# Optimization experiments

Measured on AMD Instinct MI355X. Metric: run time of the kernel, lower is better.

The kernel has to match this reference:

```python
import jax, jax.numpy as jnp
import numpy as np

D = 1024       # hidden_size
H = 16         # num_heads
DH = D // H    # d_keys = d_values = 64
FF = int(D * 2.0)  # mlp hidden
EPS = 1e-6


def _ln(t):
    # LayerNorm, elementwise_affine=False
    mu = jnp.mean(t, axis=-1, keepdims=True)
    var = jnp.mean((t - mu) ** 2, axis=-1, keepdims=True)
    return (t - mu) * jax.lax.rsqrt(var + EPS)


def setup_inputs() -> dict:
    key = jax.random.key(0)
    ks = jax.random.split(key, 16)
    B, L = 2, 2048
    s = 0.02
    return {
        "x": jax.random.normal(ks[0], (B, L, D), jnp.float32),
        "c": jax.random.normal(ks[1], (B, 1, D), jnp.float32),
        "Wq": jax.random.normal(ks[2], (D, D), jnp.float32) * s,
        "bq": jnp.zeros((D,), jnp.float32),
        "Wk": jax.random.normal(ks[3], (D, D), jnp.float32) * s,
        "bk": jnp.zeros((D,), jnp.float32),
        "Wv": jax.random.normal(ks[4], (D, D), jnp.float32) * s,
        "bv": jnp.zeros((D,), jnp.float32),
        "Wo": jax.random.normal(ks[5], (D, D), jnp.float32) * s,
        "bo": jnp.zeros((D,), jnp.float32),
        "W1": jax.random.normal(ks[6], (D, FF), jnp.float32) * s,
        "b1": jnp.zeros((FF,), jnp.float32),
        "W2": jax.random.normal(ks[7], (FF, D), jnp.float32) * s,
        "b2": jnp.zeros((D,), jnp.float32),
        "Wada": jax.random.normal(ks[8], (D, 6 * D), jnp.float32) * s,
        "bada": jnp.zeros((6 * D,), jnp.float32),
    }


def reference(x, c, Wq, bq, Wk, bk, Wv, bv, Wo, bo, W1, b1, W2, b2, Wada, bada):
    B, L, _ = x.shape
    # adaLN-Zero modulation params (dropout layers act as identity in eval)
    ada = jax.nn.silu(c) @ Wada + bada  # [B,1,6D]
    shift_msa, scale_msa, gate_msa, shift_mlp, scale_mlp, gate_mlp = jnp.split(ada, 6, axis=-1)

    # --- attention branch ---
    h = _ln(x) * (1.0 + scale_msa) + shift_msa
    q = (h @ Wq + bq).reshape(B, L, H, DH)
    k = (h @ Wk + bk).reshape(B, L, H, DH)
    v = (h @ Wv + bv).reshape(B, L, H, DH)
    scale = 1.0 / np.sqrt(DH).astype(np.float32)
    scores = jnp.einsum('blhe,bshe->bhls', q, k)  # full LxL scores, as in source
    A = jax.nn.softmax(scale * scores, axis=-1)
    out = jnp.einsum('bhls,bshd->blhd', A, v)     # [B,L,H,DH]
    # mix=True: transpose(2,1) then view(B,L,-1) -> head/position mixing reshape
    out = jnp.transpose(out, (0, 2, 1, 3)).reshape(B, L, H * DH)
    x = x + gate_msa * (out @ Wo + bo)

    # --- MLP branch (exact GELU: nn.GELU() passed as act_layer) ---
    h2 = _ln(x) * (1.0 + scale_mlp) + shift_mlp
    m = jax.nn.gelu(h2 @ W1 + b1, approximate=False) @ W2 + b2
    return x + gate_mlp * m
```

## Files before the change

kernel.cpp:

```cpp
#include <hip/hip_runtime.h>
#include <hip/hip_bf16.h>

typedef unsigned short ushort_t;
typedef __bf16 bf16x8 __attribute__((ext_vector_type(8)));
typedef float f32x4 __attribute__((ext_vector_type(4)));

typedef unsigned int u32;
typedef u32 __attribute__((address_space(1))) global_u32;
typedef u32 __attribute__((address_space(3))) lds_u32;

#define D_ 1024
#define L_ 2048
#define B_ 2
#define H_ 16
#define DH_ 64
#define FF_ 2048
#define ADA_ 6144
#define BHL_ (B_ * H_ * L_)

#define MFMA __builtin_amdgcn_mfma_f32_16x16x32_bf16

__device__ __forceinline__ ushort_t f2bf(float f) {
    union { float f; u32 u; } v; v.f = f;
    u32 r = v.u + 0x7fffu + ((v.u >> 16) & 1u);
    return (ushort_t)(r >> 16);
}

__device__ __forceinline__ u32 pk_bf16(float a, float b) {
    float2 f; f.x = a; f.y = b;
    __hip_bfloat162 t = __float22bfloat162_rn(f);
    union { __hip_bfloat162 b2; u32 u; } v; v.b2 = t; return v.u;
}

__device__ __forceinline__ void llds16(const ushort_t* src, ushort_t* dst) {
    __builtin_amdgcn_global_load_lds((global_u32*)src, (lds_u32*)dst, 16, 0, 0);
}

__global__ void transpose_w_all(
    const float* __restrict__ Wq, const float* __restrict__ Wk,
    const float* __restrict__ Wv, const float* __restrict__ Wo,
    const float* __restrict__ W1, const float* __restrict__ W2,
    ushort_t* __restrict__ Wqkv, ushort_t* __restrict__ Wo_t,
    ushort_t* __restrict__ W1_t, ushort_t* __restrict__ W2_t) {
    __shared__ float tile[64][65];
    int id = blockIdx.x;
    const float* W; ushort_t* Wt; int K, N, ntx, lid;
    if (id < 1024) {
        int which = id >> 8; lid = id & 255; K = 1024; N = 1024; ntx = 16;
        W  = which == 0 ? Wq : which == 1 ? Wk : which == 2 ? Wv : Wo;
        Wt = which == 3 ? Wo_t : Wqkv + (size_t)which * 1024 * 1024;
    } else if (id < 1536) {
        lid = id - 1024; W = W1; Wt = W1_t; K = 1024; N = 2048; ntx = 32;
    } else {
        lid = id - 1536; W = W2; Wt = W2_t; K = 2048; N = 1024; ntx = 16;
    }
    int n0 = (lid % ntx) * 64, k0 = (lid / ntx) * 64;
    int t = threadIdx.x;
    for (int p = 0; p < 4; ++p) {
        int k = p * 16 + (t >> 4), nn = (t & 15) * 4;
        float4 v = *(const float4*)(W + (size_t)(k0 + k) * N + n0 + nn);
        tile[k][nn] = v.x; tile[k][nn + 1] = v.y; tile[k][nn + 2] = v.z; tile[k][nn + 3] = v.w;
    }
    __syncthreads();
    for (int p = 0; p < 4; ++p) {
        int n = p * 16 + (t >> 4), kk = (t & 15) * 4;
        ushort4 o;
        o.x = f2bf(tile[kk][n]); o.y = f2bf(tile[kk + 1][n]);
        o.z = f2bf(tile[kk + 2][n]); o.w = f2bf(tile[kk + 3][n]);
        *(ushort4*)(Wt + (size_t)(n0 + n) * K + k0 + kk) = o;
    }
}

__global__ void transpose_v(const ushort_t* __restrict__ V, ushort_t* __restrict__ Vt) {
    __shared__ ushort_t tile[64][72];
    int bh = blockIdx.y, l0 = blockIdx.x * 64;
    const ushort_t* Vb = V + ((size_t)bh * L_ + l0) * DH_;
    ushort_t* Vtb = Vt + (size_t)bh * DH_ * L_;
    int t = threadIdx.x;
    for (int p = 0; p < 2; ++p) {
        int i = p * 32 + (t >> 3), d0 = (t & 7) * 8;
        ushort4 v0 = *(const ushort4*)(Vb + (size_t)i * DH_ + d0);
        ushort4 v1 = *(const ushort4*)(Vb + (size_t)i * DH_ + d0 + 4);
        tile[d0 + 0][i] = v0.x; tile[d0 + 1][i] = v0.y; tile[d0 + 2][i] = v0.z; tile[d0 + 3][i] = v0.w;
        tile[d0 + 4][i] = v1.x; tile[d0 + 5][i] = v1.y; tile[d0 + 6][i] = v1.z; tile[d0 + 7][i] = v1.w;
    }
    __syncthreads();
    for (int p = 0; p < 2; ++p) {
        int dh = p * 32 + (t >> 3), j0 = (t & 7) * 8;
        ushort4 o0, o1;
        o0.x = tile[dh][j0 + 0]; o0.y = tile[dh][j0 + 1]; o0.z = tile[dh][j0 + 2]; o0.w = tile[dh][j0 + 3];
        o1.x = tile[dh][j0 + 4]; o1.y = tile[dh][j0 + 5]; o1.z = tile[dh][j0 + 6]; o1.w = tile[dh][j0 + 7];
        *(ushort4*)(Vtb + (size_t)dh * L_ + l0 + j0) = o0;
        *(ushort4*)(Vtb + (size_t)dh * L_ + l0 + j0 + 4) = o1;
    }
}

__global__ void ada_gemv(const float* __restrict__ c, const float* __restrict__ Wada,
                         float* __restrict__ partial) {
    int ks = blockIdx.y;
    int j = blockIdx.x * 256 + threadIdx.x;
    __shared__ float s0[64], s1[64];
    if (threadIdx.x < 64) {
        float v = c[ks * 64 + threadIdx.x];
        s0[threadIdx.x] = v / (1.f + __expf(-v));
        v = c[D_ + ks * 64 + threadIdx.x];
        s1[threadIdx.x] = v / (1.f + __expf(-v));
    }
    __syncthreads();
    float a0 = 0.f, a1 = 0.f;
#pragma unroll 8
    for (int d = 0; d < 64; ++d) {
        float w = Wada[(size_t)(ks * 64 + d) * ADA_ + j];
        a0 = fmaf(s0[d], w, a0);
        a1 = fmaf(s1[d], w, a1);
    }
    partial[(size_t)(ks * 2 + 0) * ADA_ + j] = a0;
    partial[(size_t)(ks * 2 + 1) * ADA_ + j] = a1;
}

__global__ void ada_reduce(const float* __restrict__ partial,
                           const float* __restrict__ bada, float* __restrict__ ada) {
    int j = blockIdx.x * 256 + threadIdx.x;
    float a0 = bada[j], a1 = bada[j];
#pragma unroll
    for (int ks = 0; ks < 16; ++ks) {
        a0 += partial[(size_t)(ks * 2 + 0) * ADA_ + j];
        a1 += partial[(size_t)(ks * 2 + 1) * ADA_ + j];
    }
    ada[j] = a0;
    ada[ADA_ + j] = a1;
}

__global__ void ln_mod(const float* __restrict__ x, const float* __restrict__ ada,
                       int so, int co, ushort_t* __restrict__ out) {
    int row = blockIdx.x;
    int b = row >> 11;
    float4 v = ((const float4*)(x + (size_t)row * D_))[threadIdx.x];
    float sum = v.x + v.y + v.z + v.w;
    float sq = v.x * v.x + v.y * v.y + v.z * v.z + v.w * v.w;
    for (int off = 32; off; off >>= 1) { sum += __shfl_down(sum, off); sq += __shfl_down(sq, off); }
    __shared__ float sa[4], sb[4];
    int wave = threadIdx.x >> 6, lane = threadIdx.x & 63;
    if (lane == 0) { sa[wave] = sum; sb[wave] = sq; }
    __syncthreads();
    sum = sa[0] + sa[1] + sa[2] + sa[3];
    sq = sb[0] + sb[1] + sb[2] + sb[3];
    float mean = sum * (1.f / 1024.f);
    float var = sq * (1.f / 1024.f) - mean * mean;
    float rstd = rsqrtf(var + 1e-6f);
    int d = threadIdx.x * 4;
    const float* shf = ada + (size_t)b * ADA_ + so;
    const float* scf = ada + (size_t)b * ADA_ + co;
    uint2 ov;
    ov.x = pk_bf16((v.x - mean) * rstd * (1.f + scf[d + 0]) + shf[d + 0],
                   (v.y - mean) * rstd * (1.f + scf[d + 1]) + shf[d + 1]);
    ov.y = pk_bf16((v.z - mean) * rstd * (1.f + scf[d + 2]) + shf[d + 2],
                   (v.w - mean) * rstd * (1.f + scf[d + 3]) + shf[d + 3]);
    *(uint2*)(out + (size_t)row * D_ + d) = ov;
}

struct EpiArgs {
    const float* bias0; const float* bias1; const float* bias2;
    ushort_t* o0; ushort_t* o1; ushort_t* o2;
    const float* resid; const float* gate;
    float* fout;
};

template <int EPI>
__device__ __forceinline__ void epi_store(float v, int m, int n, int N, const EpiArgs& e) {
    if (EPI == 0) {
        int which = n >> 10, cc = n & 1023;
        const float* bias = which == 0 ? e.bias0 : which == 1 ? e.bias1 : e.bias2;
        ushort_t* ob = which == 0 ? e.o0 : which == 1 ? e.o1 : e.o2;
        v += bias[cc];
        if (which == 0) v *= 0.18033688f;
        int b = m >> 11, l = m & 2047, h = cc >> 6, dh = cc & 63;
        ob[(((size_t)(b * H_ + h) * L_) + l) * DH_ + dh] = f2bf(v);
    } else if (EPI == 1) {
        v += e.bias0[n];
        v = 0.5f * v * (1.f + erff(v * 0.70710678118f));
        e.o0[(size_t)m * N + n] = f2bf(v);
    } else {
        int b = m >> 11;
        e.fout[(size_t)m * N + n] =
            e.resid[(size_t)m * N + n] + e.gate[(size_t)b * ADA_ + n] * (v + e.bias0[n]);
    }
}

template <int EPI>
__device__ __forceinline__ void st4(const f32x4& cc, int mb, int n, int N, const EpiArgs& e) {
#pragma unroll
    for (int r = 0; r < 4; ++r) epi_store<EPI>(cc[r], mb + r, n, N, e);
}

template <int EPI>
__global__ __launch_bounds__(256, 2) void gemm_bt(
    const ushort_t* __restrict__ A, const ushort_t* __restrict__ Bt,
    int M, int N, int K, EpiArgs e) {
    __shared__ ushort_t As[128 * 64];
    __shared__ ushort_t Bs[128 * 64];
    int m0 = blockIdx.x * 128, n0 = blockIdx.y * 128;
    int tid = threadIdx.x, wave = tid >> 6, lane = tid & 63;
    int quad = lane >> 4, lc = lane & 15;
    int wm = (wave & 1) * 64, wn = (wave >> 1) * 64;
    int srow = lane >> 3, sg = lane & 7;
    int sw = lc & 7;

    const ushort_t* stp[8];
    ushort_t* stl[8];
#pragma unroll
    for (int i = 0; i < 8; ++i) {
        int chunk = wave * 8 + i;
        int c = chunk & 15;
        int row = c * 8 + srow;
        stp[i] = (chunk < 16 ? A + (size_t)(m0 + row) * K
                             : Bt + (size_t)(n0 + row) * K) + (sg ^ srow) * 8;
        stl[i] = (chunk < 16 ? As : Bs) + c * 512 + lane * 8;
    }

    f32x4 c00 = {}, c01 = {}, c02 = {}, c03 = {};
    f32x4 c10 = {}, c11 = {}, c12 = {}, c13 = {};
    f32x4 c20 = {}, c21 = {}, c22 = {}, c23 = {};
    f32x4 c30 = {}, c31 = {}, c32 = {}, c33 = {};

    for (int k0 = 0; k0 < K; k0 += 64) {
#pragma unroll
        for (int i = 0; i < 8; ++i) { llds16(stp[i], stl[i]); stp[i] += 64; }
        __syncthreads();
#pragma unroll
        for (int kk = 0; kk < 2; ++kk) {
            int off = ((kk * 4 + quad) ^ sw) * 8;
            bf16x8 a0 = *(const bf16x8*)&As[(wm +  0 + lc) * 64 + off];
            bf16x8 a1 = *(const bf16x8*)&As[(wm + 16 + lc) * 64 + off];
            bf16x8 a2 = *(const bf16x8*)&As[(wm + 32 + lc) * 64 + off];
            bf16x8 a3 = *(const bf16x8*)&As[(wm + 48 + lc) * 64 + off];
            bf16x8 b0 = *(const bf16x8*)&Bs[(wn +  0 + lc) * 64 + off];
            bf16x8 b1 = *(const bf16x8*)&Bs[(wn + 16 + lc) * 64 + off];
            bf16x8 b2 = *(const bf16x8*)&Bs[(wn + 32 + lc) * 64 + off];
            bf16x8 b3 = *(const bf16x8*)&Bs[(wn + 48 + lc) * 64 + off];
            c00 = MFMA(a0, b0, c00, 0, 0, 0); c01 = MFMA(a0, b1, c01, 0, 0, 0);
            c02 = MFMA(a0, b2, c02, 0, 0, 0); c03 = MFMA(a0, b3, c03, 0, 0, 0);
            c10 = MFMA(a1, b0, c10, 0, 0, 0); c11 = MFMA(a1, b1, c11, 0, 0, 0);
            c12 = MFMA(a1, b2, c12, 0, 0, 0); c13 = MFMA(a1, b3, c13, 0, 0, 0);
            c20 = MFMA(a2, b0, c20, 0, 0, 0); c21 = MFMA(a2, b1, c21, 0, 0, 0);
            c22 = MFMA(a2, b2, c22, 0, 0, 0); c23 = MFMA(a2, b3, c23, 0, 0, 0);
            c30 = MFMA(a3, b0, c30, 0, 0, 0); c31 = MFMA(a3, b1, c31, 0, 0, 0);
            c32 = MFMA(a3, b2, c32, 0, 0, 0); c33 = MFMA(a3, b3, c33, 0, 0, 0);
        }
        __syncthreads();
    }

    int mb = m0 + wm + quad * 4, nb = n0 + wn + lc;
    st4<EPI>(c00, mb +  0, nb +  0, N, e); st4<EPI>(c01, mb +  0, nb + 16, N, e);
    st4<EPI>(c02, mb +  0, nb + 32, N, e); st4<EPI>(c03, mb +  0, nb + 48, N, e);
    st4<EPI>(c10, mb + 16, nb +  0, N, e); st4<EPI>(c11, mb + 16, nb + 16, N, e);
    st4<EPI>(c12, mb + 16, nb + 32, N, e); st4<EPI>(c13, mb + 16, nb + 48, N, e);
    st4<EPI>(c20, mb + 32, nb +  0, N, e); st4<EPI>(c21, mb + 32, nb + 16, N, e);
    st4<EPI>(c22, mb + 32, nb + 32, N, e); st4<EPI>(c23, mb + 32, nb + 48, N, e);
    st4<EPI>(c30, mb + 48, nb +  0, N, e); st4<EPI>(c31, mb + 48, nb + 16, N, e);
    st4<EPI>(c32, mb + 48, nb + 32, N, e); st4<EPI>(c33, mb + 48, nb + 48, N, e);
}

template <int EPI>
__global__ __launch_bounds__(256, 2) void gemm_bt64(
    const ushort_t* __restrict__ A, const ushort_t* __restrict__ Bt,
    int M, int N, int K, EpiArgs e) {
    __shared__ ushort_t As[64 * 64];
    __shared__ ushort_t Bs[128 * 64];
    int m0 = blockIdx.x * 64, n0 = blockIdx.y * 128;
    int tid = threadIdx.x, wave = tid >> 6, lane = tid & 63;
    int quad = lane >> 4, lc = lane & 15;
    int wn = wave * 32;
    int srow = lane >> 3, sg = lane & 7;
    int sw = lc & 7;

    const ushort_t* stp[6];
    ushort_t* stl[6];
#pragma unroll
    for (int i = 0; i < 6; ++i) {
        int chunk = wave * 6 + i;
        if (chunk < 8) {
            int row = chunk * 8 + srow;
            stp[i] = A + (size_t)(m0 + row) * K + (sg ^ srow) * 8;
            stl[i] = &As[chunk * 512 + lane * 8];
        } else {
            int c = chunk - 8;
            int row = c * 8 + srow;
            stp[i] = Bt + (size_t)(n0 + row) * K + (sg ^ srow) * 8;
            stl[i] = &Bs[c * 512 + lane * 8];
        }
    }

    f32x4 c00 = {}, c01 = {};
    f32x4 c10 = {}, c11 = {};
    f32x4 c20 = {}, c21 = {};
    f32x4 c30 = {}, c31 = {};

    for (int k0 = 0; k0 < K; k0 += 64) {
#pragma unroll
        for (int i = 0; i < 6; ++i) { llds16(stp[i], stl[i]); stp[i] += 64; }
        __syncthreads();
#pragma unroll
        for (int kk = 0; kk < 2; ++kk) {
            int off = ((kk * 4 + quad) ^ sw) * 8;
            bf16x8 a0 = *(const bf16x8*)&As[( 0 + lc) * 64 + off];
            bf16x8 a1 = *(const bf16x8*)&As[(16 + lc) * 64 + off];
            bf16x8 a2 = *(const bf16x8*)&As[(32 + lc) * 64 + off];
            bf16x8 a3 = *(const bf16x8*)&As[(48 + lc) * 64 + off];
            bf16x8 b0 = *(const bf16x8*)&Bs[(wn +  0 + lc) * 64 + off];
            bf16x8 b1 = *(const bf16x8*)&Bs[(wn + 16 + lc) * 64 + off];
            c00 = MFMA(a0, b0, c00, 0, 0, 0); c01 = MFMA(a0, b1, c01, 0, 0, 0);
            c10 = MFMA(a1, b0, c10, 0, 0, 0); c11 = MFMA(a1, b1, c11, 0, 0, 0);
            c20 = MFMA(a2, b0, c20, 0, 0, 0); c21 = MFMA(a2, b1, c21, 0, 0, 0);
            c30 = MFMA(a3, b0, c30, 0, 0, 0); c31 = MFMA(a3, b1, c31, 0, 0, 0);
        }
        __syncthreads();
    }

    int mb = m0 + quad * 4, nb = n0 + wn + lc;
    st4<EPI>(c00, mb +  0, nb + 0, N, e); st4<EPI>(c01, mb +  0, nb + 16, N, e);
    st4<EPI>(c10, mb + 16, nb + 0, N, e); st4<EPI>(c11, mb + 16, nb + 16, N, e);
    st4<EPI>(c20, mb + 32, nb + 0, N, e); st4<EPI>(c21, mb + 32, nb + 16, N, e);
    st4<EPI>(c30, mb + 48, nb + 0, N, e); st4<EPI>(c31, mb + 48, nb + 16, N, e);
}

__global__ __launch_bounds__(256, 2) void attn(
    const ushort_t* __restrict__ Q, const ushort_t* __restrict__ Kx,
    const ushort_t* __restrict__ Vt,
    ushort_t* __restrict__ Op0, ushort_t* __restrict__ Op1,
    ushort_t* __restrict__ Op2, ushort_t* __restrict__ Op3,
    float* __restrict__ lsum) {
    __shared__ ushort_t Ks[128 * 64];
    __shared__ ushort_t Vs[64 * 128];
    int id = blockIdx.x;
    int bh = ((id & 7) << 2) + ((id >> 3) & 3);
    int quarter = (id >> 5) & 3;
    int qt = id >> 7;
    const ushort_t* Qg = Q + ((size_t)bh * L_ + qt * 128) * DH_;
    const ushort_t* Kg = Kx + (size_t)bh * L_ * DH_;
    const ushort_t* Vg = Vt + (size_t)bh * DH_ * L_;
    int tid = threadIdx.x, wave = tid >> 6, lane = tid & 63;
    int quad = lane >> 4, lc = lane & 15;
    int sw = lc & 7;
    int srow = lane >> 3, sg = lane & 7;

    const ushort_t* stp[8];
    ushort_t* stl[8];
    int stinc;
    if (wave < 2) {
        stinc = 128 * DH_;
#pragma unroll
        for (int i = 0; i < 8; ++i) {
            int chunk = wave * 8 + i;
            int slot = chunk * 8 + srow;
            int s5 = slot & 31;
            int sig = (slot & ~31) + ((s5 & 15) >> 2) * 8 + (s5 & 3) + (s5 >> 4) * 4;
            stp[i] = Kg + (size_t)(quarter * 512 + sig) * DH_ + (sg ^ srow) * 8;
            stl[i] = &Ks[chunk * 512 + lane * 8];
        }
    } else {
        stinc = 128;
#pragma unroll
        for (int i = 0; i < 8; ++i) {
            int c2 = (wave - 2) * 8 + i;
            int row = c2 * 4 + (lane >> 4);
            int g = (lane & 15) ^ (row & 15);
            stp[i] = Vg + (size_t)row * L_ + quarter * 512 + g * 8;
            stl[i] = &Vs[c2 * 512 + lane * 8];
        }
    }

    const ushort_t* qp = Qg + (size_t)(wave * 32 + lc) * DH_ + quad * 8;
    bf16x8 q00 = *(const bf16x8*)(qp);
    bf16x8 q01 = *(const bf16x8*)(qp + 32);
    bf16x8 q10 = *(const bf16x8*)(qp + 16 * DH_);
    bf16x8 q11 = *(const bf16x8*)(qp + 16 * DH_ + 32);

    union { u32 u[4]; bf16x8 v; } ones;
    ones.u[0] = ones.u[1] = ones.u[2] = ones.u[3] = 0x3F803F80u;

    f32x4 o00 = {}, o01 = {}, o02 = {}, o03 = {};
    f32x4 o10 = {}, o11 = {}, o12 = {}, o13 = {};
    f32x4 osum0 = {}, osum1 = {};

    for (int t = 0; t < 4; ++t) {
#pragma unroll
        for (int i = 0; i < 8; ++i) { llds16(stp[i], stl[i]); stp[i] += stinc; }
        __syncthreads();

        f32x4 s[2][8];
        __builtin_amdgcn_s_setprio(1);
#pragma unroll
        for (int kk = 0; kk < 2; ++kk) {
            int off = ((kk * 4 + quad) ^ sw) * 8;
            bf16x8 aq0 = kk == 0 ? q00 : q01;
            bf16x8 aq1 = kk == 0 ? q10 : q11;
#pragma unroll
            for (int ni = 0; ni < 8; ++ni) {
                bf16x8 bk = *(const bf16x8*)&Ks[(ni * 16 + lc) * 64 + off];
                if (kk == 0) {
                    f32x4 z = {0.f, 0.f, 0.f, 0.f};
                    s[0][ni] = MFMA(bk, aq0, z, 0, 0, 0);
                    s[1][ni] = MFMA(bk, aq1, z, 0, 0, 0);
                } else {
                    s[0][ni] = MFMA(bk, aq0, s[0][ni], 0, 0, 0);
                    s[1][ni] = MFMA(bk, aq1, s[1][ni], 0, 0, 0);
                }
            }
        }
        __builtin_amdgcn_s_setprio(0);

        u32 px[2][8], py[2][8];
#pragma unroll
        for (int pi = 0; pi < 2; ++pi) {
#pragma unroll
            for (int ni = 0; ni < 8; ++ni) {
                float p0 = __builtin_amdgcn_exp2f(s[pi][ni][0]);
                float p1 = __builtin_amdgcn_exp2f(s[pi][ni][1]);
                float p2 = __builtin_amdgcn_exp2f(s[pi][ni][2]);
                float p3 = __builtin_amdgcn_exp2f(s[pi][ni][3]);
                px[pi][ni] = pk_bf16(p0, p1);
                py[pi][ni] = pk_bf16(p2, p3);
            }
        }

        __builtin_amdgcn_s_setprio(1);
#pragma unroll
        for (int kk = 0; kk < 4; ++kk) {
            int gq = kk * 4 + quad;
            bf16x8 bv0 = *(const bf16x8*)&Vs[( 0 + lc) * 128 + ((gq ^ lc) * 8)];
            bf16x8 bv1 = *(const bf16x8*)&Vs[(16 + lc) * 128 + ((gq ^ lc) * 8)];
            bf16x8 bv2 = *(const bf16x8*)&Vs[(32 + lc) * 128 + ((gq ^ lc) * 8)];
            bf16x8 bv3 = *(const bf16x8*)&Vs[(48 + lc) * 128 + ((gq ^ lc) * 8)];
            union { u32 u[4]; bf16x8 v; } a0, a1;
            a0.u[0] = px[0][2 * kk]; a0.u[1] = py[0][2 * kk];
            a0.u[2] = px[0][2 * kk + 1]; a0.u[3] = py[0][2 * kk + 1];
            a1.u[0] = px[1][2 * kk]; a1.u[1] = py[1][2 * kk];
            a1.u[2] = px[1][2 * kk + 1]; a1.u[3] = py[1][2 * kk + 1];
            o00 = MFMA(a0.v, bv0, o00, 0, 0, 0); o01 = MFMA(a0.v, bv1, o01, 0, 0, 0);
            o02 = MFMA(a0.v, bv2, o02, 0, 0, 0); o03 = MFMA(a0.v, bv3, o03, 0, 0, 0);
            o10 = MFMA(a1.v, bv0, o10, 0, 0, 0); o11 = MFMA(a1.v, bv1, o11, 0, 0, 0);
            o12 = MFMA(a1.v, bv2, o12, 0, 0, 0); o13 = MFMA(a1.v, bv3, o13, 0, 0, 0);
            osum0 = MFMA(a0.v, ones.v, osum0, 0, 0, 0);
            osum1 = MFMA(a1.v, ones.v, osum1, 0, 0, 0);
        }
        __builtin_amdgcn_s_setprio(0);
        __syncthreads();
    }

    ushort_t* Op = quarter == 0 ? Op0 : quarter == 1 ? Op1 : quarter == 2 ? Op2 : Op3;
#pragma unroll
    for (int pi = 0; pi < 2; ++pi) {
#pragma unroll
        for (int nio = 0; nio < 4; ++nio) {
            const f32x4& ov = pi == 0 ? (nio == 0 ? o00 : nio == 1 ? o01 : nio == 2 ? o02 : o03)
                                      : (nio == 0 ? o10 : nio == 1 ? o11 : nio == 2 ? o12 : o13);
#pragma unroll
            for (int r = 0; r < 4; ++r) {
                int row = qt * 128 + wave * 32 + pi * 16 + quad * 4 + r;
                Op[((size_t)bh * L_ + row) * DH_ + nio * 16 + lc] = f2bf(ov[r]);
            }
        }
    }
    if (lc == 0) {
        int base = qt * 128 + wave * 32 + quad * 4;
#pragma unroll
        for (int r = 0; r < 4; ++r) {
            lsum[(size_t)quarter * BHL_ + (size_t)bh * L_ + base + r] = osum0[r];
            lsum[(size_t)quarter * BHL_ + (size_t)bh * L_ + base + 16 + r] = osum1[r];
        }
    }
}

__global__ void attn_merge(const ushort_t* __restrict__ Op0,
                           const ushort_t* __restrict__ Op1,
                           const ushort_t* __restrict__ Op2,
                           const ushort_t* __restrict__ Op3,
                           const float* __restrict__ lsum,
                           ushort_t* __restrict__ O) {
    int gid = blockIdx.x * 256 + threadIdx.x;
    int row = gid >> 3, j = gid & 7;
    float inv = 1.f / (lsum[row] + lsum[BHL_ + row] +
                       lsum[2 * BHL_ + row] + lsum[3 * BHL_ + row]);
    bf16x8 v0 = *(const bf16x8*)(Op0 + (size_t)row * DH_ + j * 8);
    bf16x8 v1 = *(const bf16x8*)(Op1 + (size_t)row * DH_ + j * 8);
    bf16x8 v2 = *(const bf16x8*)(Op2 + (size_t)row * DH_ + j * 8);
    bf16x8 v3 = *(const bf16x8*)(Op3 + (size_t)row * DH_ + j * 8);
    uint4 o;
    float r0, r1;
#pragma unroll
    for (int k = 0; k < 4; ++k) {
        r0 = ((float)v0[2 * k] + (float)v1[2 * k] + (float)v2[2 * k] + (float)v3[2 * k]) * inv;
        r1 = ((float)v0[2 * k + 1] + (float)v1[2 * k + 1] + (float)v2[2 * k + 1] + (float)v3[2 * k + 1]) * inv;
        ((u32*)&o)[k] = pk_bf16(r0, r1);
    }
    *(uint4*)(O + (size_t)row * DH_ + j * 8) = o;
}

extern "C" void kernel_launch(void* const* d_in, const int* in_sizes, int n_in,
                              void* d_out, int out_size, void* d_ws, size_t ws_size,
                              hipStream_t stream) {
    (void)in_sizes; (void)n_in; (void)out_size; (void)ws_size;
    const float* x    = (const float*)d_in[0];
    const float* c    = (const float*)d_in[1];
    const float* Wq   = (const float*)d_in[2];
    const float* bq   = (const float*)d_in[3];
    const float* Wk   = (const float*)d_in[4];
    const float* bk   = (const float*)d_in[5];
    const float* Wv   = (const float*)d_in[6];
    const float* bv   = (const float*)d_in[7];
    const float* Wo   = (const float*)d_in[8];
    const float* bo   = (const float*)d_in[9];
    const float* W1   = (const float*)d_in[10];
    const float* b1   = (const float*)d_in[11];
    const float* W2   = (const float*)d_in[12];
    const float* b2   = (const float*)d_in[13];
    const float* Wada = (const float*)d_in[14];
    const float* bada = (const float*)d_in[15];

    char* w = (char*)d_ws;
    float*    ada  = (float*)(w + 0);
    ushort_t* Wqkv = (ushort_t*)(w + 49152);
    ushort_t* Wo_t = (ushort_t*)(w + 6340608);
    ushort_t* W1_t = (ushort_t*)(w + 8437760);
    ushort_t* W2_t = (ushort_t*)(w + 12632064);
    ushort_t* h    = (ushort_t*)(w + 16826368);
    ushort_t* Qb   = (ushort_t*)(w + 25214976);
    ushort_t* Kb   = (ushort_t*)(w + 33603584);
    ushort_t* Vb   = (ushort_t*)(w + 41992192);
    ushort_t* Vtb  = (ushort_t*)(w + 50380800);
    float*    x1   = (float*)(w + 58769408);
    ushort_t* Ob   = Qb;
    ushort_t* m1   = Qb;
    float*    lsb  = (float*)Wqkv;
    float*    adap = (float*)Vtb;
    ushort_t* p2   = (ushort_t*)x1;
    ushort_t* p3   = (ushort_t*)((char*)x1 + 8388608);

    const int M = B_ * L_;

    transpose_w_all<<<2048, 256, 0, stream>>>(Wq, Wk, Wv, Wo, W1, W2,
                                              Wqkv, Wo_t, W1_t, W2_t);

    ada_gemv<<<dim3(24, 16), 256, 0, stream>>>(c, Wada, adap);
    ada_reduce<<<24, 256, 0, stream>>>(adap, bada, ada);
    ln_mod<<<M, 256, 0, stream>>>(x, ada, 0, 1024, h);

    EpiArgs e0 = {bq, bk, bv, Qb, Kb, Vb, nullptr, nullptr, nullptr};
    gemm_bt<0><<<dim3(32, 24), 256, 0, stream>>>(h, Wqkv, M, 3072, D_, e0);

    transpose_v<<<dim3(32, 32), 256, 0, stream>>>(Vb, Vtb);

    attn<<<2048, 256, 0, stream>>>(Qb, Kb, Vtb, Vb, h, p2, p3, lsb);
    attn_merge<<<2048, 256, 0, stream>>>(Vb, h, p2, p3, lsb, Ob);

    EpiArgs e1 = {bo, nullptr, nullptr, nullptr, nullptr, nullptr, x, ada + 2048, x1};
    gemm_bt64<2><<<dim3(64, 8), 256, 0, stream>>>(Ob, Wo_t, M, D_, D_, e1);

    ln_mod<<<M, 256, 0, stream>>>(x1, ada, 3072, 4096, h);

    EpiArgs e2 = {b1, nullptr, nullptr, m1, nullptr, nullptr, nullptr, nullptr, nullptr};
    gemm_bt64<1><<<dim3(64, 16), 256, 0, stream>>>(h, W1_t, M, FF_, D_, e2);

    EpiArgs e3 = {b2, nullptr, nullptr, nullptr, nullptr, nullptr, x1, ada + 5120, (float*)d_out};
    gemm_bt64<2><<<dim3(64, 8), 256, 0, stream>>>(m1, W2_t, M, D_, FF_, e3);
}
```

Before: 321.4 us.

## Write V transposed from QKV GEMM epilogue and drop split-K attention merge

The QKV GEMM epilogue now writes V straight into the transposed [bh, dh, L] layout with 4-wide stores, so the separate transpose_v kernel goes away. Attention no longer splits the key dimension into four quarters with partial outputs and a merge kernel. Each block loops over all 2048 keys and normalizes by the row sum in its own epilogue. This removes two launches and the partial-output and row-sum traffic, but the attention grid shrinks from 2048 to 512 blocks, which lowers parallelism and lengthens each block's serial loop.

```diff
diff --git a/kernel.cpp b/kernel.cpp
--- a/kernel.cpp
+++ b/kernel.cpp
@@ -68,30 +68,6 @@
         o.x = f2bf(tile[kk][n]); o.y = f2bf(tile[kk + 1][n]);
         o.z = f2bf(tile[kk + 2][n]); o.w = f2bf(tile[kk + 3][n]);
         *(ushort4*)(Wt + (size_t)(n0 + n) * K + k0 + kk) = o;
-    }
-}
-
-__global__ void transpose_v(const ushort_t* __restrict__ V, ushort_t* __restrict__ Vt) {
-    __shared__ ushort_t tile[64][72];
-    int bh = blockIdx.y, l0 = blockIdx.x * 64;
-    const ushort_t* Vb = V + ((size_t)bh * L_ + l0) * DH_;
-    ushort_t* Vtb = Vt + (size_t)bh * DH_ * L_;
-    int t = threadIdx.x;
-    for (int p = 0; p < 2; ++p) {
-        int i = p * 32 + (t >> 3), d0 = (t & 7) * 8;
-        ushort4 v0 = *(const ushort4*)(Vb + (size_t)i * DH_ + d0);
-        ushort4 v1 = *(const ushort4*)(Vb + (size_t)i * DH_ + d0 + 4);
-        tile[d0 + 0][i] = v0.x; tile[d0 + 1][i] = v0.y; tile[d0 + 2][i] = v0.z; tile[d0 + 3][i] = v0.w;
-        tile[d0 + 4][i] = v1.x; tile[d0 + 5][i] = v1.y; tile[d0 + 6][i] = v1.z; tile[d0 + 7][i] = v1.w;
-    }
-    __syncthreads();
-    for (int p = 0; p < 2; ++p) {
-        int dh = p * 32 + (t >> 3), j0 = (t & 7) * 8;
-        ushort4 o0, o1;
-        o0.x = tile[dh][j0 + 0]; o0.y = tile[dh][j0 + 1]; o0.z = tile[dh][j0 + 2]; o0.w = tile[dh][j0 + 3];
-        o1.x = tile[dh][j0 + 4]; o1.y = tile[dh][j0 + 5]; o1.z = tile[dh][j0 + 6]; o1.w = tile[dh][j0 + 7];
-        *(ushort4*)(Vtb + (size_t)dh * L_ + l0 + j0) = o0;
-        *(ushort4*)(Vtb + (size_t)dh * L_ + l0 + j0 + 4) = o1;
     }
 }
 
@@ -170,8 +146,8 @@
 __device__ __forceinline__ void epi_store(float v, int m, int n, int N, const EpiArgs& e) {
     if (EPI == 0) {
         int which = n >> 10, cc = n & 1023;
-        const float* bias = which == 0 ? e.bias0 : which == 1 ? e.bias1 : e.bias2;
-        ushort_t* ob = which == 0 ? e.o0 : which == 1 ? e.o1 : e.o2;
+        const float* bias = which == 0 ? e.bias0 : e.bias1;
+        ushort_t* ob = which == 0 ? e.o0 : e.o1;
         v += bias[cc];
         if (which == 0) v *= 0.18033688f;
         int b = m >> 11, l = m & 2047, h = cc >> 6, dh = cc & 63;
@@ -189,6 +165,16 @@
 
 template <int EPI>
 __device__ __forceinline__ void st4(const f32x4& cc, int mb, int n, int N, const EpiArgs& e) {
+    if (EPI == 0 && n >= 2048) {
+        int ccn = n & 1023;
+        float b4 = e.bias2[ccn];
+        int b = mb >> 11, l0 = mb & 2047, h = ccn >> 6, dh = ccn & 63;
+        ushort4 o;
+        o.x = f2bf(cc[0] + b4); o.y = f2bf(cc[1] + b4);
+        o.z = f2bf(cc[2] + b4); o.w = f2bf(cc[3] + b4);
+        *(ushort4*)(e.o2 + ((size_t)(b * H_ + h) * DH_ + dh) * L_ + l0) = o;
+        return;
+    }
 #pragma unroll
     for (int r = 0; r < 4; ++r) epi_store<EPI>(cc[r], mb + r, n, N, e);
 }
@@ -326,16 +312,12 @@
 
 __global__ __launch_bounds__(256, 2) void attn(
     const ushort_t* __restrict__ Q, const ushort_t* __restrict__ Kx,
-    const ushort_t* __restrict__ Vt,
-    ushort_t* __restrict__ Op0, ushort_t* __restrict__ Op1,
-    ushort_t* __restrict__ Op2, ushort_t* __restrict__ Op3,
-    float* __restrict__ lsum) {
+    const ushort_t* __restrict__ Vt, ushort_t* __restrict__ O) {
     __shared__ ushort_t Ks[128 * 64];
     __shared__ ushort_t Vs[64 * 128];
     int id = blockIdx.x;
     int bh = ((id & 7) << 2) + ((id >> 3) & 3);
-    int quarter = (id >> 5) & 3;
-    int qt = id >> 7;
+    int qt = id >> 5;
     const ushort_t* Qg = Q + ((size_t)bh * L_ + qt * 128) * DH_;
     const ushort_t* Kg = Kx + (size_t)bh * L_ * DH_;
     const ushort_t* Vg = Vt + (size_t)bh * DH_ * L_;
@@ -355,7 +337,7 @@
             int slot = chunk * 8 + srow;
             int s5 = slot & 31;
             int sig = (slot & ~31) + ((s5 & 15) >> 2) * 8 + (s5 & 3) + (s5 >> 4) * 4;
-            stp[i] = Kg + (size_t)(quarter * 512 + sig) * DH_ + (sg ^ srow) * 8;
+            stp[i] = Kg + (size_t)sig * DH_ + (sg ^ srow) * 8;
             stl[i] = &Ks[chunk * 512 + lane * 8];
         }
     } else {
@@ -365,7 +347,7 @@
             int c2 = (wave - 2) * 8 + i;
             int row = c2 * 4 + (lane >> 4);
             int g = (lane & 15) ^ (row & 15);
-            stp[i] = Vg + (size_t)row * L_ + quarter * 512 + g * 8;
+            stp[i] = Vg + (size_t)row * L_ + g * 8;
             stl[i] = &Vs[c2 * 512 + lane * 8];
         }
     }
@@ -383,7 +365,7 @@
     f32x4 o10 = {}, o11 = {}, o12 = {}, o13 = {};
     f32x4 osum0 = {}, osum1 = {};
 
-    for (int t = 0; t < 4; ++t) {
+    for (int t = 0; t < 16; ++t) {
 #pragma unroll
         for (int i = 0; i < 8; ++i) { llds16(stp[i], stl[i]); stp[i] += stinc; }
         __syncthreads();
@@ -448,9 +430,12 @@
         __syncthreads();
     }
 
-    ushort_t* Op = quarter == 0 ? Op0 : quarter == 1 ? Op1 : quarter == 2 ? Op2 : Op3;
+    f32x4 inv0, inv1;
+#pragma unroll
+    for (int r = 0; r < 4; ++r) { inv0[r] = 1.f / osum0[r]; inv1[r] = 1.f / osum1[r]; }
 #pragma unroll
     for (int pi = 0; pi < 2; ++pi) {
+        const f32x4& iv = pi == 0 ? inv0 : inv1;
 #pragma unroll
         for (int nio = 0; nio < 4; ++nio) {
             const f32x4& ov = pi == 0 ? (nio == 0 ? o00 : nio == 1 ? o01 : nio == 2 ? o02 : o03)
@@ -458,43 +443,10 @@
 #pragma unroll
             for (int r = 0; r < 4; ++r) {
                 int row = qt * 128 + wave * 32 + pi * 16 + quad * 4 + r;
-                Op[((size_t)bh * L_ + row) * DH_ + nio * 16 + lc] = f2bf(ov[r]);
+                O[((size_t)bh * L_ + row) * DH_ + nio * 16 + lc] = f2bf(ov[r] * iv[r]);
             }
         }
     }
-    if (lc == 0) {
-        int base = qt * 128 + wave * 32 + quad * 4;
-#pragma unroll
-        for (int r = 0; r < 4; ++r) {
-            lsum[(size_t)quarter * BHL_ + (size_t)bh * L_ + base + r] = osum0[r];
-            lsum[(size_t)quarter * BHL_ + (size_t)bh * L_ + base + 16 + r] = osum1[r];
-        }
-    }
-}
-
-__global__ void attn_merge(const ushort_t* __restrict__ Op0,
-                           const ushort_t* __restrict__ Op1,
-                           const ushort_t* __restrict__ Op2,
-                           const ushort_t* __restrict__ Op3,
-                           const float* __restrict__ lsum,
-                           ushort_t* __restrict__ O) {
-    int gid = blockIdx.x * 256 + threadIdx.x;
-    int row = gid >> 3, j = gid & 7;
-    float inv = 1.f / (lsum[row] + lsum[BHL_ + row] +
-                       lsum[2 * BHL_ + row] + lsum[3 * BHL_ + row]);
-    bf16x8 v0 = *(const bf16x8*)(Op0 + (size_t)row * DH_ + j * 8);
-    bf16x8 v1 = *(const bf16x8*)(Op1 + (size_t)row * DH_ + j * 8);
-    bf16x8 v2 = *(const bf16x8*)(Op2 + (size_t)row * DH_ + j * 8);
-    bf16x8 v3 = *(const bf16x8*)(Op3 + (size_t)row * DH_ + j * 8);
-    uint4 o;
-    float r0, r1;
-#pragma unroll
-    for (int k = 0; k < 4; ++k) {
-        r0 = ((float)v0[2 * k] + (float)v1[2 * k] + (float)v2[2 * k] + (float)v3[2 * k]) * inv;
-        r1 = ((float)v0[2 * k + 1] + (float)v1[2 * k + 1] + (float)v2[2 * k + 1] + (float)v3[2 * k + 1]) * inv;
-        ((u32*)&o)[k] = pk_bf16(r0, r1);
-    }
-    *(uint4*)(O + (size_t)row * DH_ + j * 8) = o;
 }
 
 extern "C" void kernel_launch(void* const* d_in, const int* in_sizes, int n_in,
@@ -527,15 +479,11 @@
     ushort_t* h    = (ushort_t*)(w + 16826368);
     ushort_t* Qb   = (ushort_t*)(w + 25214976);
     ushort_t* Kb   = (ushort_t*)(w + 33603584);
-    ushort_t* Vb   = (ushort_t*)(w + 41992192);
+    ushort_t* Ob   = (ushort_t*)(w + 41992192);
     ushort_t* Vtb  = (ushort_t*)(w + 50380800);
     float*    x1   = (float*)(w + 58769408);
-    ushort_t* Ob   = Qb;
     ushort_t* m1   = Qb;
-    float*    lsb  = (float*)Wqkv;
     float*    adap = (float*)Vtb;
-    ushort_t* p2   = (ushort_t*)x1;
-    ushort_t* p3   = (ushort_t*)((char*)x1 + 8388608);
 
     const int M = B_ * L_;
 
@@ -546,13 +494,10 @@
     ada_reduce<<<24, 256, 0, stream>>>(adap, bada, ada);
     ln_mod<<<M, 256, 0, stream>>>(x, ada, 0, 1024, h);
 
-    EpiArgs e0 = {bq, bk, bv, Qb, Kb, Vb, nullptr, nullptr, nullptr};
+    EpiArgs e0 = {bq, bk, bv, Qb, Kb, Vtb, nullptr, nullptr, nullptr};
     gemm_bt<0><<<dim3(32, 24), 256, 0, stream>>>(h, Wqkv, M, 3072, D_, e0);
 
-    transpose_v<<<dim3(32, 32), 256, 0, stream>>>(Vb, Vtb);
-
-    attn<<<2048, 256, 0, stream>>>(Qb, Kb, Vtb, Vb, h, p2, p3, lsb);
-    attn_merge<<<2048, 256, 0, stream>>>(Vb, h, p2, p3, lsb, Ob);
+    attn<<<512, 256, 0, stream>>>(Qb, Kb, Vtb, Ob);
 
     EpiArgs e1 = {bo, nullptr, nullptr, nullptr, nullptr, nullptr, x, ada + 2048, x1};
     gemm_bt64<2><<<dim3(64, 8), 256, 0, stream>>>(Ob, Wo_t, M, D_, D_, e1);
```

Result: faster. 314.7 us (-2.1%).
